# Kernel optimization log

Hardware: AMD Instinct MI355X
Metric: run time of the kernel (lower is better)

The kernel has to match this reference:

```python
import jax, jax.numpy as jnp
import numpy as np

GAMMA = 10.0  # kernel bandwidth (init arg gamma)

def setup_inputs() -> dict:
    key = jax.random.key(0)
    k1, k2, k3, k4 = jax.random.split(key, 4)
    n_train, n_test, d, n_cls = 16384, 8192, 3072, 10
    return {
        "x_train": jax.random.normal(k1, (n_train, d), dtype=jnp.float32),
        "y_train": jax.random.normal(k2, (n_train, n_cls), dtype=jnp.float32),
        "x_test": jax.random.normal(k3, (n_test, d), dtype=jnp.float32),
        "M": jax.random.normal(k4, (d, d), dtype=jnp.float32),
    }

def reference(x_train, y_train, x_test, M):
    # Mahalanobis squared distances: ||s||_M^2 - 2 s M c^T + ||c||_M^2
    sM = x_train @ M                              # [n_train, d]
    s_norm2 = (sM * x_train).sum(-1)              # [n_train]
    c_norm2 = ((x_test @ M) * x_test).sum(-1)     # [n_test]
    d2 = (-2.0) * (sM @ x_test.T) + s_norm2[:, None] + c_norm2[None, :]
    dist = jnp.sqrt(jnp.clip(d2, 0.0))            # laplacian uses non-squared dist
    K = jnp.exp(dist * (-1.0 / GAMMA))            # [n_train, n_test]
    Kt = K.T                                      # [n_test, n_train]
    normalized = Kt / Kt.sum(axis=1, keepdims=True)
    out = normalized @ y_train                    # [n_test, n_cls]
    return (out, M)
```

## Files before the change

kernel.cpp:

```cpp
#include <hip/hip_runtime.h>
#include <hip/hip_bf16.h>

#define D_DIM 3072
#define NTRAIN 16384
#define NTEST 8192

typedef __attribute__((ext_vector_type(4))) float f32x4;
typedef __attribute__((ext_vector_type(4))) int i32x4;
typedef __attribute__((ext_vector_type(8))) int i32x8;

__device__ __forceinline__ unsigned short f2bf(float f) {
  union { float f; unsigned u; } x; x.f = f;
  unsigned r = x.u + 0x7FFFu + ((x.u >> 16) & 1u);
  return (unsigned short)(r >> 16);
}

__device__ __forceinline__ float bf2f(unsigned short b) {
  union { unsigned u; float f; } x; x.u = ((unsigned)b) << 16;
  return x.f;
}

__device__ __forceinline__ i32x8 cmb(i32x4 lo, i32x4 hi) {
  i32x8 r;
  r[0] = lo[0]; r[1] = lo[1]; r[2] = lo[2]; r[3] = lo[3];
  r[4] = hi[0]; r[5] = hi[1]; r[6] = hi[2]; r[7] = hi[3];
  return r;
}

__device__ __forceinline__ void gload16(const void* g, void* l) {
  __builtin_amdgcn_global_load_lds(
      (const __attribute__((address_space(1))) void*)g,
      (__attribute__((address_space(3))) void*)l, 16, 0, 0);
}

__device__ __forceinline__ void swz_tile(int& tileY, int& tileX) {
  const int gx = gridDim.x, gy = gridDim.y;
  const int L = blockIdx.y * gx + blockIdx.x;
  const int q = (gx * gy) >> 3;
  const int s = (L & 7) * q + (L >> 3);
  const int sid = s >> 6;
  const int t = s & 63;
  const int scols = gx >> 3;
  const int sy = sid / scols, sx = sid - sy * scols;
  tileY = sy * 8 + (t >> 3);
  tileX = sx * 8 + (t & 7);
}

__device__ __forceinline__ void swz_lin(int& tileY, int& tileX) {
  const int gx = gridDim.x;
  const int nwg = gx * gridDim.y;
  const int L = blockIdx.y * gx + blockIdx.x;
  const int s = (L & 7) * (nwg >> 3) + (L >> 3);
  tileY = s / gx;
  tileX = s - tileY * gx;
}

__global__ void k_convert8(const float* __restrict__ in, unsigned char* __restrict__ out, long n8) {
  long i = (long)blockIdx.x * blockDim.x + threadIdx.x;
  long stride = (long)gridDim.x * blockDim.x;
  for (; i < n8; i += stride) {
    float4 a = reinterpret_cast<const float4*>(in)[i * 2];
    float4 b = reinterpret_cast<const float4*>(in)[i * 2 + 1];
    int w0 = __builtin_amdgcn_cvt_pk_fp8_f32(a.x, a.y, 0, false);
    w0 = __builtin_amdgcn_cvt_pk_fp8_f32(a.z, a.w, w0, true);
    int w1 = __builtin_amdgcn_cvt_pk_fp8_f32(b.x, b.y, 0, false);
    w1 = __builtin_amdgcn_cvt_pk_fp8_f32(b.z, b.w, w1, true);
    reinterpret_cast<int2*>(out)[i] = make_int2(w0, w1);
  }
}

__global__ void k_copy4(const float4* __restrict__ in, float4* __restrict__ out, long n4) {
  long i = (long)blockIdx.x * blockDim.x + threadIdx.x;
  long stride = (long)gridDim.x * blockDim.x;
  for (; i < n4; i += stride) out[i] = in[i];
}

__global__ void k_transpose_fp8(const float* __restrict__ M, unsigned char* __restrict__ Mt) {
  __shared__ float t[32][33];
  int bx = blockIdx.x * 32, by = blockIdx.y * 32;
  int tx = threadIdx.x, ty = threadIdx.y;
#pragma unroll
  for (int i = 0; i < 32; i += 8)
    t[ty + i][tx] = M[(size_t)(by + ty + i) * D_DIM + bx + tx];
  __syncthreads();
#pragma unroll
  for (int i = 0; i < 32; i += 8) {
    float v = t[tx][ty + i];
    int p = __builtin_amdgcn_cvt_pk_fp8_f32(v, v, 0, false);
    Mt[(size_t)(bx + ty + i) * D_DIM + by + tx] = (unsigned char)(p & 0xFF);
  }
}

__device__ __forceinline__ void mainloop4ph(const unsigned char* __restrict__ ga,
                                            const unsigned char* __restrict__ gb,
                                            unsigned char* As, unsigned char* Bs,
                                            int aRow0, int bRow0, int lhi, int tid,
                                            f32x4 acc[8][4]) {
  const int nt = D_DIM / 128;
#pragma unroll
  for (int j = 0; j < 4; ++j) {
    gload16(ga + (size_t)j * 64 * D_DIM, As + j * 8192 + tid * 16);
    gload16(gb + (size_t)j * 64 * D_DIM, Bs + j * 8192 + tid * 16);
  }
  const int g0 = lhi, g1 = lhi ^ 4;
  for (int t = 0; t < nt; ++t) {
    const int p = t & 1;
    const unsigned char* Ac = As + p * 32768;
    const unsigned char* Bc = Bs + p * 32768;
    unsigned char* An = As + (p ^ 1) * 32768;
    unsigned char* Bn = Bs + (p ^ 1) * 32768;
    const bool stage = (t + 1 < nt);
    const int k1 = (t + 1) * 128;
    asm volatile("s_waitcnt vmcnt(0)" ::: "memory");
    __builtin_amdgcn_s_barrier();
    __builtin_amdgcn_sched_barrier(0);
    if (stage) {
#pragma unroll
      for (int j = 0; j < 4; ++j) {
        gload16(ga + (size_t)j * 64 * D_DIM + k1, An + j * 8192 + tid * 16);
        gload16(gb + (size_t)j * 64 * D_DIM + k1, Bn + j * 8192 + tid * 16);
      }
    }
    i32x8 b8[4];
#pragma unroll
    for (int n = 0; n < 4; ++n) {
      const int row = bRow0 + n * 16;
      const int f = row & 7;
      i32x4 lo = *reinterpret_cast<const i32x4*>(&Bc[row * 128 + ((g0 ^ f) * 16)]);
      i32x4 hi = *reinterpret_cast<const i32x4*>(&Bc[row * 128 + ((g1 ^ f) * 16)]);
      b8[n] = cmb(lo, hi);
    }
#pragma unroll
    for (int q = 0; q < 4; ++q) {
      i32x8 a80, a81;
      {
        const int r0 = aRow0 + q * 32;
        const int f0 = r0 & 7;
        i32x4 lo = *reinterpret_cast<const i32x4*>(&Ac[r0 * 128 + ((g0 ^ f0) * 16)]);
        i32x4 hi = *reinterpret_cast<const i32x4*>(&Ac[r0 * 128 + ((g1 ^ f0) * 16)]);
        a80 = cmb(lo, hi);
        const int r1 = r0 + 16;
        const int f1 = r1 & 7;
        lo = *reinterpret_cast<const i32x4*>(&Ac[r1 * 128 + ((g0 ^ f1) * 16)]);
        hi = *reinterpret_cast<const i32x4*>(&Ac[r1 * 128 + ((g1 ^ f1) * 16)]);
        a81 = cmb(lo, hi);
      }
      __builtin_amdgcn_s_setprio(1);
#pragma unroll
      for (int n = 0; n < 4; ++n) {
        acc[q * 2][n] = __builtin_amdgcn_mfma_scale_f32_16x16x128_f8f6f4(
            a80, b8[n], acc[q * 2][n], 0, 0, 0, 127, 0, 127);
        acc[q * 2 + 1][n] = __builtin_amdgcn_mfma_scale_f32_16x16x128_f8f6f4(
            a81, b8[n], acc[q * 2 + 1][n], 0, 0, 0, 127, 0, 127);
      }
      __builtin_amdgcn_s_setprio(0);
      __builtin_amdgcn_sched_barrier(0);
    }
  }
}

template <bool WRITE_SM>
__global__ __launch_bounds__(512, 2) void k_gemm_xm8(const unsigned char* __restrict__ X8,
                                                     const unsigned char* __restrict__ Mt8,
                                                     const float* __restrict__ Xf,
                                                     unsigned char* __restrict__ smOut,
                                                     float* __restrict__ norm) {
  __shared__ unsigned char As[2 * 256 * 128], Bs[2 * 256 * 128];
  const int tid = threadIdx.x, lane = tid & 63, wave = tid >> 6;
  const int wm = wave >> 2, wn = wave & 3;
  const int l15 = lane & 15, lhi = lane >> 4;
  int tileY, tileX;
  swz_lin(tileY, tileX);
  const int rowBase = tileY * 256, colBase = tileX * 256;
  const int srow = tid >> 3, ssl = tid & 7;
  const unsigned char* ga = X8 + (size_t)(rowBase + srow) * D_DIM + ((ssl ^ (srow & 7)) * 16);
  const unsigned char* gb = Mt8 + (size_t)(colBase + srow) * D_DIM + ((ssl ^ (srow & 7)) * 16);
  f32x4 acc[8][4] = {};
  mainloop4ph(ga, gb, As, Bs, wm * 128 + l15, wn * 64 + l15, lhi, tid, acc);
  __syncthreads();

  const int c0 = colBase + wn * 64 + l15;
#pragma unroll
  for (int m = 0; m < 8; ++m) {
#pragma unroll
    for (int r = 0; r < 4; ++r) {
      const size_t grow = rowBase + wm * 128 + m * 16 + lhi * 4 + r;
      float v = 0.f;
#pragma unroll
      for (int n = 0; n < 4; ++n) {
        float a = acc[m][n][r];
        const int gcol = c0 + n * 16;
        v += a * Xf[grow * D_DIM + gcol];
        if (WRITE_SM) {
          int pk = __builtin_amdgcn_cvt_pk_fp8_f32(a, a, 0, false);
          smOut[grow * D_DIM + gcol] = (unsigned char)(pk & 0xFF);
        }
      }
      v += __shfl_xor(v, 1); v += __shfl_xor(v, 2);
      v += __shfl_xor(v, 4); v += __shfl_xor(v, 8);
      if ((lane & 15) == 0) atomicAdd(&norm[grow], v);
    }
  }
}

__global__ __launch_bounds__(512, 2) void k_gemm_cross(const unsigned char* __restrict__ sM8,
                                                       const unsigned char* __restrict__ xte8h,
                                                       const float* __restrict__ sn2,
                                                       const float* __restrict__ cn2h,
                                                       unsigned short* __restrict__ S) {
  __shared__ unsigned char As[2 * 256 * 128], Bs[2 * 256 * 128];
  const int tid = threadIdx.x, lane = tid & 63, wave = tid >> 6;
  const int wm = wave >> 2, wn = wave & 3;
  const int l15 = lane & 15, lhi = lane >> 4;
  int tileY, tileX;
  swz_tile(tileY, tileX);
  const int rowBase = tileY * 256, colBase = tileX * 256;
  const int srow = tid >> 3, ssl = tid & 7;
  const unsigned char* ga = sM8 + (size_t)(rowBase + srow) * D_DIM + ((ssl ^ (srow & 7)) * 16);
  const unsigned char* gb = xte8h + (size_t)(colBase + srow) * D_DIM + ((ssl ^ (srow & 7)) * 16);
  const int bRow0 = wn * 64 + l15;
  f32x4 acc[8][4] = {};
  mainloop4ph(ga, gb, As, Bs, wm * 128 + l15, bRow0, lhi, tid, acc);
  __syncthreads();

  float* snlds = reinterpret_cast<float*>(As);
  if (tid < 256) snlds[tid] = sn2[rowBase + tid];
  __syncthreads();
  float cn[4];
#pragma unroll
  for (int n = 0; n < 4; ++n) cn[n] = cn2h[colBase + bRow0 + n * 16];
#pragma unroll
  for (int m = 0; m < 8; ++m) {
#pragma unroll
    for (int r = 0; r < 4; ++r) {
      const int lrow = wm * 128 + m * 16 + lhi * 4 + r;
      const float sn = snlds[lrow];
      const size_t grow = rowBase + lrow;
#pragma unroll
      for (int n = 0; n < 4; ++n) {
        float d2 = sn + cn[n] - 2.f * acc[m][n][r];
        float kv = exp2f(-0.14426950408889634f * sqrtf(fmaxf(d2, 0.f)));
        S[grow * 4096 + colBase + bRow0 + n * 16] = f2bf(kv);
      }
    }
  }
}

__global__ __launch_bounds__(256) void k_out(const unsigned short* __restrict__ S,
                                             const float* __restrict__ Y,
                                             float* __restrict__ part, int halfBase) {
  __shared__ float ylds[256 * 10];
  const int tid = threadIdx.x;
  const int sBase = blockIdx.y * 256;
  const int tloc = blockIdx.x * 256 + tid;
  const int tglob = halfBase + tloc;
  for (int i = tid; i < 2560; i += 256) ylds[i] = Y[(size_t)sBase * 10 + i];
  __syncthreads();
  float num[10] = {0, 0, 0, 0, 0, 0, 0, 0, 0, 0};
  float den = 0.f;
  for (int s = 0; s < 256; ++s) {
    float kv = bf2f(S[(size_t)(sBase + s) * 4096 + tloc]);
    const float* yr = &ylds[s * 10];
#pragma unroll
    for (int c = 0; c < 10; ++c) num[c] += kv * yr[c];
    den += kv;
  }
#pragma unroll
  for (int c = 0; c < 10; ++c)
    part[((size_t)blockIdx.y * 11 + c) * NTEST + tglob] = num[c];
  part[((size_t)blockIdx.y * 11 + 10) * NTEST + tglob] = den;
}

__global__ void k_reduce(const float* __restrict__ part, float* __restrict__ out) {
  int t = blockIdx.x * blockDim.x + threadIdx.x;
  float num[10] = {0, 0, 0, 0, 0, 0, 0, 0, 0, 0};
  float den = 0.f;
  for (int it = 0; it < NTRAIN / 256; ++it) {
    const float* p = part + (size_t)it * 11 * NTEST + t;
#pragma unroll
    for (int c = 0; c < 10; ++c) num[c] += p[(size_t)c * NTEST];
    den += p[(size_t)10 * NTEST];
  }
  float inv = 1.f / den;
#pragma unroll
  for (int c = 0; c < 10; ++c) out[(size_t)t * 10 + c] = num[c] * inv;
}

extern "C" void kernel_launch(void* const* d_in, const int* in_sizes, int n_in,
                              void* d_out, int out_size, void* d_ws, size_t ws_size,
                              hipStream_t stream) {
  const float* x_train = (const float*)d_in[0];
  const float* y_train = (const float*)d_in[1];
  const float* x_test  = (const float*)d_in[2];
  const float* M       = (const float*)d_in[3];
  float* out = (float*)d_out;

  char* ws = (char*)d_ws;
  unsigned char*  xtr8 = (unsigned char*)(ws + 0);
  unsigned char*  xte8 = (unsigned char*)(ws + 50331648);
  unsigned char*  Mt8  = (unsigned char*)(ws + 75497472);
  unsigned char*  sM8  = (unsigned char*)(ws + 84934656);
  float* s_n2 = (float*)(ws + 135266304);
  float* c_n2 = (float*)(ws + 135331840);
  float* part = (float*)(ws + 135364608);
  unsigned short* S = (unsigned short*)(ws + 158433280);

  hipMemsetAsync(ws + 135266304, 0, 98304, stream);

  k_convert8<<<1024, 256, 0, stream>>>(x_train, xtr8, (long)NTRAIN * D_DIM / 8);
  k_convert8<<<1024, 256, 0, stream>>>(x_test, xte8, (long)NTEST * D_DIM / 8);
  k_transpose_fp8<<<dim3(96, 96), dim3(32, 8), 0, stream>>>(M, Mt8);
  k_copy4<<<2048, 256, 0, stream>>>((const float4*)M, (float4*)(out + 81920),
                                    (long)D_DIM * D_DIM / 4);

  k_gemm_xm8<true><<<dim3(12, 64), 512, 0, stream>>>(xtr8, Mt8, x_train, sM8, s_n2);
  k_gemm_xm8<false><<<dim3(12, 32), 512, 0, stream>>>(xte8, Mt8, x_test, nullptr, c_n2);

  for (int h = 0; h < 2; ++h) {
    k_gemm_cross<<<dim3(16, 64), 512, 0, stream>>>(
        sM8, xte8 + (size_t)h * 4096 * D_DIM, s_n2, c_n2 + h * 4096, S);
    k_out<<<dim3(16, 64), 256, 0, stream>>>(S, y_train, part, h * 4096);
  }
  k_reduce<<<32, 256, 0, stream>>>(part, out);
}
```

Baseline: 1.077 ms.

## Load B operand directly from global memory into registers, skip LDS staging

```diff
diff --git a/kernel.cpp b/kernel.cpp
--- a/kernel.cpp
+++ b/kernel.cpp
@@ -91,72 +91,61 @@
   }
 }
 
-__device__ __forceinline__ void mainloop4ph(const unsigned char* __restrict__ ga,
-                                            const unsigned char* __restrict__ gb,
-                                            unsigned char* As, unsigned char* Bs,
-                                            int aRow0, int bRow0, int lhi, int tid,
-                                            f32x4 acc[8][4]) {
+__device__ __forceinline__ void mainloopBG(const unsigned char* __restrict__ ga,
+                                           const unsigned char* __restrict__ gBrow,
+                                           unsigned char* As,
+                                           int aRow0, int lhi, int tid,
+                                           f32x4 acc[8][4]) {
   const int nt = D_DIM / 128;
-#pragma unroll
-  for (int j = 0; j < 4; ++j) {
+  const int g0 = lhi, g1 = lhi ^ 4;
+#pragma unroll
+  for (int j = 0; j < 4; ++j)
     gload16(ga + (size_t)j * 64 * D_DIM, As + j * 8192 + tid * 16);
-    gload16(gb + (size_t)j * 64 * D_DIM, Bs + j * 8192 + tid * 16);
-  }
-  const int g0 = lhi, g1 = lhi ^ 4;
+
+#define RDA(Ac, q, H)                                                                \
+  cmb(*reinterpret_cast<const i32x4*>(                                               \
+          &(Ac)[(aRow0 + (q) * 32 + (H) * 16) * 128 +                                \
+                ((g0 ^ ((aRow0 + (q) * 32 + (H) * 16) & 7)) * 16)]),                 \
+      *reinterpret_cast<const i32x4*>(                                               \
+          &(Ac)[(aRow0 + (q) * 32 + (H) * 16) * 128 +                                \
+                ((g1 ^ ((aRow0 + (q) * 32 + (H) * 16) & 7)) * 16)]))
+
   for (int t = 0; t < nt; ++t) {
     const int p = t & 1;
     const unsigned char* Ac = As + p * 32768;
-    const unsigned char* Bc = Bs + p * 32768;
     unsigned char* An = As + (p ^ 1) * 32768;
-    unsigned char* Bn = Bs + (p ^ 1) * 32768;
-    const bool stage = (t + 1 < nt);
-    const int k1 = (t + 1) * 128;
     asm volatile("s_waitcnt vmcnt(0)" ::: "memory");
     __builtin_amdgcn_s_barrier();
     __builtin_amdgcn_sched_barrier(0);
-    if (stage) {
-#pragma unroll
-      for (int j = 0; j < 4; ++j) {
+    if (t + 1 < nt) {
+      const int k1 = (t + 1) * 128;
+#pragma unroll
+      for (int j = 0; j < 4; ++j)
         gload16(ga + (size_t)j * 64 * D_DIM + k1, An + j * 8192 + tid * 16);
-        gload16(gb + (size_t)j * 64 * D_DIM + k1, Bn + j * 8192 + tid * 16);
-      }
     }
+    const unsigned char* pB = gBrow + (size_t)t * 128;
     i32x8 b8[4];
 #pragma unroll
-    for (int n = 0; n < 4; ++n) {
-      const int row = bRow0 + n * 16;
-      const int f = row & 7;
-      i32x4 lo = *reinterpret_cast<const i32x4*>(&Bc[row * 128 + ((g0 ^ f) * 16)]);
-      i32x4 hi = *reinterpret_cast<const i32x4*>(&Bc[row * 128 + ((g1 ^ f) * 16)]);
-      b8[n] = cmb(lo, hi);
-    }
+    for (int n = 0; n < 4; ++n)
+      b8[n] = cmb(*reinterpret_cast<const i32x4*>(pB + (size_t)n * 16 * D_DIM + g0 * 16),
+                  *reinterpret_cast<const i32x4*>(pB + (size_t)n * 16 * D_DIM + g1 * 16));
+    __builtin_amdgcn_sched_barrier(0);
 #pragma unroll
     for (int q = 0; q < 4; ++q) {
-      i32x8 a80, a81;
-      {
-        const int r0 = aRow0 + q * 32;
-        const int f0 = r0 & 7;
-        i32x4 lo = *reinterpret_cast<const i32x4*>(&Ac[r0 * 128 + ((g0 ^ f0) * 16)]);
-        i32x4 hi = *reinterpret_cast<const i32x4*>(&Ac[r0 * 128 + ((g1 ^ f0) * 16)]);
-        a80 = cmb(lo, hi);
-        const int r1 = r0 + 16;
-        const int f1 = r1 & 7;
-        lo = *reinterpret_cast<const i32x4*>(&Ac[r1 * 128 + ((g0 ^ f1) * 16)]);
-        hi = *reinterpret_cast<const i32x4*>(&Ac[r1 * 128 + ((g1 ^ f1) * 16)]);
-        a81 = cmb(lo, hi);
-      }
+      i32x8 a0 = RDA(Ac, q, 0), a1 = RDA(Ac, q, 1);
       __builtin_amdgcn_s_setprio(1);
 #pragma unroll
       for (int n = 0; n < 4; ++n) {
         acc[q * 2][n] = __builtin_amdgcn_mfma_scale_f32_16x16x128_f8f6f4(
-            a80, b8[n], acc[q * 2][n], 0, 0, 0, 127, 0, 127);
+            a0, b8[n], acc[q * 2][n], 0, 0, 0, 127, 0, 127);
         acc[q * 2 + 1][n] = __builtin_amdgcn_mfma_scale_f32_16x16x128_f8f6f4(
-            a81, b8[n], acc[q * 2 + 1][n], 0, 0, 0, 127, 0, 127);
+            a1, b8[n], acc[q * 2 + 1][n], 0, 0, 0, 127, 0, 127);
       }
       __builtin_amdgcn_s_setprio(0);
       __builtin_amdgcn_sched_barrier(0);
     }
   }
+#undef RDA
 }
 
 template <bool WRITE_SM>
@@ -165,7 +154,7 @@
                                                      const float* __restrict__ Xf,
                                                      unsigned char* __restrict__ smOut,
                                                      float* __restrict__ norm) {
-  __shared__ unsigned char As[2 * 256 * 128], Bs[2 * 256 * 128];
+  __shared__ unsigned char As[2 * 256 * 128];
   const int tid = threadIdx.x, lane = tid & 63, wave = tid >> 6;
   const int wm = wave >> 2, wn = wave & 3;
   const int l15 = lane & 15, lhi = lane >> 4;
@@ -174,9 +163,9 @@
   const int rowBase = tileY * 256, colBase = tileX * 256;
   const int srow = tid >> 3, ssl = tid & 7;
   const unsigned char* ga = X8 + (size_t)(rowBase + srow) * D_DIM + ((ssl ^ (srow & 7)) * 16);
-  const unsigned char* gb = Mt8 + (size_t)(colBase + srow) * D_DIM + ((ssl ^ (srow & 7)) * 16);
+  const unsigned char* gBrow = Mt8 + (size_t)(colBase + wn * 64 + l15) * D_DIM;
   f32x4 acc[8][4] = {};
-  mainloop4ph(ga, gb, As, Bs, wm * 128 + l15, wn * 64 + l15, lhi, tid, acc);
+  mainloopBG(ga, gBrow, As, wm * 128 + l15, lhi, tid, acc);
   __syncthreads();
 
   const int c0 = colBase + wn * 64 + l15;
@@ -208,7 +197,7 @@
                                                        const float* __restrict__ sn2,
                                                        const float* __restrict__ cn2h,
                                                        unsigned short* __restrict__ S) {
-  __shared__ unsigned char As[2 * 256 * 128], Bs[2 * 256 * 128];
+  __shared__ unsigned char As[2 * 256 * 128];
   const int tid = threadIdx.x, lane = tid & 63, wave = tid >> 6;
   const int wm = wave >> 2, wn = wave & 3;
   const int l15 = lane & 15, lhi = lane >> 4;
@@ -217,10 +206,10 @@
   const int rowBase = tileY * 256, colBase = tileX * 256;
   const int srow = tid >> 3, ssl = tid & 7;
   const unsigned char* ga = sM8 + (size_t)(rowBase + srow) * D_DIM + ((ssl ^ (srow & 7)) * 16);
-  const unsigned char* gb = xte8h + (size_t)(colBase + srow) * D_DIM + ((ssl ^ (srow & 7)) * 16);
   const int bRow0 = wn * 64 + l15;
+  const unsigned char* gBrow = xte8h + (size_t)(colBase + bRow0) * D_DIM;
   f32x4 acc[8][4] = {};
-  mainloop4ph(ga, gb, As, Bs, wm * 128 + l15, bRow0, lhi, tid, acc);
+  mainloopBG(ga, gBrow, As, wm * 128 + l15, lhi, tid, acc);
   __syncthreads();
 
   float* snlds = reinterpret_cast<float*>(As);
```

Result: slower. 1.366 ms (+26.9%).
